# Optimization experiments

Measured on AMD Instinct MI355X. Metric: run time of the kernel, lower is better.

The kernel has to match this reference:

```python
import jax, jax.numpy as jnp
import numpy as np

D_MODEL = 1024
D_FF = 8192
N_ELEM = 64            # d2 (elements per block)
D1 = D_FF // N_ELEM    # 128 block rows
BATCH = 2048


def setup_inputs() -> dict:
    key = jax.random.key(0)
    k1, k2, k3, k4, k5 = jax.random.split(key, 5)
    # xavier-uniform-like init for w1 (d_model, d_ff) -> view (d_model, d1, d2)
    bound1 = float(np.sqrt(6.0 / (D_MODEL + D_FF)))
    w1 = jax.random.uniform(k1, (D_MODEL, D1, N_ELEM), jnp.float32, -bound1, bound1)
    # w2 (d_ff, d_model) -> view (d2, d1, d_model); kernel_scaling=True multiplies by sqrt(d2)
    w2 = jax.random.uniform(k2, (N_ELEM, D1, D_MODEL), jnp.float32, -bound1, bound1)
    w2 = w2 * (N_ELEM ** 0.5)
    b2 = jax.random.normal(k3, (D_MODEL,), jnp.float32)
    x = jax.random.normal(k4, (BATCH, D_MODEL), jnp.float32)
    quant_mask = jax.random.randint(k5, (BATCH, D1), 0, N_ELEM, jnp.int32)
    return {"quant_mask": quant_mask, "x": x, "w1": w1, "w2": w2, "b2": b2}


def reference(quant_mask, x, w1, w2, b2):
    # predict-mode path of SparseFFMain (multiply_by_controller_output=False)
    d1 = w1.shape[1]
    w1p = jnp.transpose(w1, (1, 2, 0))   # (d1, d2, d_model)
    w2p = jnp.transpose(w2, (1, 0, 2))   # (d1, d2, d_model)
    rows = jnp.arange(d1)[None, :]        # (1, d1) broadcasts over batch
    # per-sample gathered expert sub-blocks: (B, d1, d_model)
    w = w1p[rows, quant_mask]
    v = w2p[rows, quant_mask]
    mid = jnp.einsum('bd,bjd->bj', x, w)   # (B, d1)
    relu = jax.nn.relu(mid)
    res = jnp.einsum('bj,bjd->bd', relu, v) + b2  # (B, d_model)
    return (quant_mask, res)
```

## Files before the change

### kernel.cpp

```cpp
#include <hip/hip_runtime.h>

#define D_MODEL 1024
#define D_FF    8192
#define N_ELEM  64
#define D1      128
#define BATCH   2048
#define B_T     8
#define NJT     8
#define JT      16

typedef unsigned short u16;
typedef unsigned int   u32;
typedef _Float16 h2    __attribute__((ext_vector_type(2)));
typedef float    f32x4 __attribute__((ext_vector_type(4)));
typedef u32      u32x2 __attribute__((ext_vector_type(2)));
typedef u32      u32x4 __attribute__((ext_vector_type(4)));

__device__ __forceinline__ h2 as_h2(u32 u) { union { u32 i; h2 h; } c; c.i = u; return c.h; }
__device__ __forceinline__ u32 pkh(float a, float b) {
    union { h2 h; u32 u; } c; c.h.x = (_Float16)a; c.h.y = (_Float16)b; return c.u;
}
__device__ __forceinline__ u16 f2h(float f) {
    union { _Float16 h; u16 u; } c; c.h = (_Float16)f; return c.u;
}
__device__ __forceinline__ f32x4 ntload4(const float* p) {
    return __builtin_nontemporal_load((const f32x4*)p);
}
__device__ __forceinline__ float dot2(u32 a, u32 b, float c) {
#if __has_builtin(__builtin_amdgcn_fdot2)
    return __builtin_amdgcn_fdot2(as_h2(a), as_h2(b), c, false);
#else
    const h2 ha = as_h2(a), hb = as_h2(b);
    c = fmaf((float)ha.x, (float)hb.x, c);
    return fmaf((float)ha.y, (float)hb.y, c);
#endif
}
__device__ __forceinline__ float dot8(uint4 w, uint4 q, float c) {
    c = dot2(w.x, q.x, c);
    c = dot2(w.y, q.y, c);
    c = dot2(w.z, q.z, c);
    c = dot2(w.w, q.w, c);
    return c;
}

#define TW1_BLOCKS ((D_FF / 64) * (D_MODEL / 64))
__global__ __launch_bounds__(256) void prep_weights(const float* __restrict__ w1,
                                                    u16* __restrict__ w1h,
                                                    const float* __restrict__ w2,
                                                    u16* __restrict__ w2h) {
    __shared__ float tile[64][65];
    if (blockIdx.x < TW1_BLOCKS) {
        const int c0 = (blockIdx.x & (D_FF / 64 - 1)) * 64;
        const int d0 = (blockIdx.x >> 7) * 64;
        const int tx = threadIdx.x & 15;
        const int ty = threadIdx.x >> 4;
#pragma unroll
        for (int r = 0; r < 4; ++r) {
            const int row = ty * 4 + r;
            const float4 v = *(const float4*)(w1 + (size_t)(d0 + row) * D_FF + c0 + tx * 4);
            tile[row][tx * 4 + 0] = v.x;
            tile[row][tx * 4 + 1] = v.y;
            tile[row][tx * 4 + 2] = v.z;
            tile[row][tx * 4 + 3] = v.w;
        }
        __syncthreads();
#pragma unroll
        for (int r = 0; r < 4; ++r) {
            const int c = ty * 4 + r;
            ushort4 o;
            o.x = f2h(tile[tx * 4 + 0][c]);
            o.y = f2h(tile[tx * 4 + 1][c]);
            o.z = f2h(tile[tx * 4 + 2][c]);
            o.w = f2h(tile[tx * 4 + 3][c]);
            *(ushort4*)(w1h + (size_t)(c0 + c) * D_MODEL + d0 + tx * 4) = o;
        }
    } else {
        const size_t i = ((size_t)(blockIdx.x - TW1_BLOCKS) * 256 + threadIdx.x) * 8;
        const float4 a = *(const float4*)(w2 + i);
        const float4 b = *(const float4*)(w2 + i + 4);
        ushort4 oa, ob;
        oa.x = f2h(a.x); oa.y = f2h(a.y); oa.z = f2h(a.z); oa.w = f2h(a.w);
        ob.x = f2h(b.x); ob.y = f2h(b.y); ob.z = f2h(b.z); ob.w = f2h(b.w);
        *(ushort4*)(w2h + i)     = oa;
        *(ushort4*)(w2h + i + 4) = ob;
    }
}

__global__ __launch_bounds__(256) void sparse_ff_jt(const int* __restrict__ mask,
                                                    const float* __restrict__ x,
                                                    const u16* __restrict__ w1h_,
                                                    const u16* __restrict__ w2h_,
                                                    u16* __restrict__ part) {
    const _Float16* w1h = (const _Float16*)w1h_;
    const _Float16* w2h = (const _Float16*)w2h_;
    __shared__ u16   x_lds[B_T][D_MODEL];
    __shared__ float r_lds[B_T][JT];
    __shared__ int   m_lds[B_T][JT];

    const int jt = blockIdx.x & (NJT - 1);
    const int b0 = (blockIdx.x >> 3) * B_T;
    const int t = threadIdx.x;
    const int wave = t >> 6;
    const int lane = t & 63;

#pragma unroll
    for (int r = 0; r < B_T; ++r) {
        const f32x4 v = ntload4(x + (size_t)(b0 + r) * D_MODEL + t * 4);
        u32x2 o; o.x = pkh(v.x, v.y); o.y = pkh(v.z, v.w);
        *(u32x2*)&x_lds[r][t * 4] = o;
    }
    if (t < B_T * JT) {
        m_lds[t >> 4][t & 15] = mask[(b0 + (t >> 4)) * D1 + jt * JT + (t & 15)];
    }
    __syncthreads();

#pragma unroll
    for (int rep = 0; rep < 2; ++rep) {
        const int bi = wave * 2 + rep;
        const uint4 xA = *(const uint4*)&x_lds[bi][lane * 8];
        const uint4 xB = *(const uint4*)&x_lds[bi][512 + lane * 8];

#pragma unroll
        for (int jj = 0; jj < JT; jj += 4) {
            const int j0 = jt * JT + jj;
            const _Float16* c0 = w1h + (size_t)(((j0 + 0) << 6) + m_lds[bi][jj + 0]) * D_MODEL + lane * 8;
            const _Float16* c1 = w1h + (size_t)(((j0 + 1) << 6) + m_lds[bi][jj + 1]) * D_MODEL + lane * 8;
            const _Float16* c2 = w1h + (size_t)(((j0 + 2) << 6) + m_lds[bi][jj + 2]) * D_MODEL + lane * 8;
            const _Float16* c3 = w1h + (size_t)(((j0 + 3) << 6) + m_lds[bi][jj + 3]) * D_MODEL + lane * 8;
            const uint4 a0 = *(const uint4*)c0;
            const uint4 a1 = *(const uint4*)c1;
            const uint4 a2 = *(const uint4*)c2;
            const uint4 a3 = *(const uint4*)c3;
            const uint4 e0 = *(const uint4*)(c0 + 512);
            const uint4 e1 = *(const uint4*)(c1 + 512);
            const uint4 e2 = *(const uint4*)(c2 + 512);
            const uint4 e3 = *(const uint4*)(c3 + 512);

            float s0 = dot8(a0, xA, 0.f); s0 = dot8(e0, xB, s0);
            float s1 = dot8(a1, xA, 0.f); s1 = dot8(e1, xB, s1);
            float s2 = dot8(a2, xA, 0.f); s2 = dot8(e2, xB, s2);
            float s3 = dot8(a3, xA, 0.f); s3 = dot8(e3, xB, s3);

#pragma unroll
            for (int off = 32; off; off >>= 1) {
                s0 += __shfl_down(s0, off);
                s1 += __shfl_down(s1, off);
                s2 += __shfl_down(s2, off);
                s3 += __shfl_down(s3, off);
            }
            if (lane == 0) {
                r_lds[bi][jj + 0] = fmaxf(s0, 0.f);
                r_lds[bi][jj + 1] = fmaxf(s1, 0.f);
                r_lds[bi][jj + 2] = fmaxf(s2, 0.f);
                r_lds[bi][jj + 3] = fmaxf(s3, 0.f);
            }
        }
    }
    __syncthreads();

    const int halfsel = t >> 7;
    const int d0q = (t & 127) * 8;
#pragma unroll
    for (int p = 0; p < 4; ++p) {
        const int bi = p * 2 + halfsel;
        float a0 = 0.f, a1 = 0.f, a2 = 0.f, a3 = 0.f;
        float a4 = 0.f, a5 = 0.f, a6 = 0.f, a7 = 0.f;
#pragma unroll
        for (int jj = 0; jj < JT; ++jj) {
            const float r = r_lds[bi][jj];
            const _Float16* row = w2h
                + (size_t)(m_lds[bi][jj] * D1 + jt * JT + jj) * D_MODEL + d0q;
            const uint4 v = *(const uint4*)row;
            const h2 q0 = as_h2(v.x), q1 = as_h2(v.y);
            const h2 q2 = as_h2(v.z), q3 = as_h2(v.w);
            a0 = fmaf(r, (float)q0.x, a0); a1 = fmaf(r, (float)q0.y, a1);
            a2 = fmaf(r, (float)q1.x, a2); a3 = fmaf(r, (float)q1.y, a3);
            a4 = fmaf(r, (float)q2.x, a4); a5 = fmaf(r, (float)q2.y, a5);
            a6 = fmaf(r, (float)q3.x, a6); a7 = fmaf(r, (float)q3.y, a7);
        }
        u32x4 o;
        o.x = pkh(a0, a1); o.y = pkh(a2, a3);
        o.z = pkh(a4, a5); o.w = pkh(a6, a7);
        u16* pp = part + ((size_t)jt * BATCH + (b0 + bi)) * D_MODEL + d0q;
        __builtin_nontemporal_store(o, (u32x4*)pp);
    }
}

__global__ __launch_bounds__(256) void reduce_partials(const int* __restrict__ mask,
                                                       const float* __restrict__ b2,
                                                       const u16* __restrict__ part,
                                                       float* __restrict__ out) {
    const int b = blockIdx.x;
    const int t = threadIdx.x;
    if (t < D1) out[(size_t)b * D1 + t] = (float)mask[b * D1 + t];

    const int d0 = t * 4;
    const float4 bv = *(const float4*)(b2 + d0);
    float a0 = bv.x, a1 = bv.y, a2 = bv.z, a3 = bv.w;
#pragma unroll
    for (int jt = 0; jt < NJT; ++jt) {
        const uint2 v = *(const uint2*)(part + ((size_t)jt * BATCH + b) * D_MODEL + d0);
        const h2 p0 = as_h2(v.x), p1 = as_h2(v.y);
        a0 += (float)p0.x; a1 += (float)p0.y;
        a2 += (float)p1.x; a3 += (float)p1.y;
    }
    *(float4*)(out + (size_t)BATCH * D1 + (size_t)b * D_MODEL + d0) =
        make_float4(a0, a1, a2, a3);
}

__global__ __launch_bounds__(256) void sparse_ff_f32_raw(const int* __restrict__ mask,
                                                         const float* __restrict__ x,
                                                         const float* __restrict__ w1,
                                                         const float* __restrict__ w2,
                                                         const float* __restrict__ b2,
                                                         float* __restrict__ out) {
    __shared__ float x_lds[D_MODEL];
    __shared__ float relu_lds[D1];
    __shared__ int   m_lds[D1];
    const int b = blockIdx.x, t = threadIdx.x;
    const int wave = t >> 6, lane = t & 63;
    *(float4*)&x_lds[t * 4] = *(const float4*)(x + (size_t)b * D_MODEL + t * 4);
    if (t < D1) {
        const int mv = mask[b * D1 + t];
        m_lds[t] = mv;
        out[(size_t)b * D1 + t] = (float)mv;
    }
    __syncthreads();
    for (int jj = 0; jj < 32; ++jj) {
        const int j = wave * 32 + jj;
        const int m = m_lds[j];
        float acc = 0.f;
#pragma unroll
        for (int c = 0; c < 16; ++c) {
            const int d = c * 64 + lane;
            acc = fmaf(w1[(size_t)d * D_FF + j * N_ELEM + m], x_lds[d], acc);
        }
#pragma unroll
        for (int off = 32; off; off >>= 1) acc += __shfl_down(acc, off);
        if (lane == 0) relu_lds[j] = fmaxf(acc, 0.f);
    }
    __syncthreads();
    const int dm0 = t * 4;
    const float4 bv = *(const float4*)(b2 + dm0);
    float a0 = bv.x, a1 = bv.y, a2 = bv.z, a3 = bv.w;
    for (int j = 0; j < D1; ++j) {
        const float r = relu_lds[j];
        if (r > 0.f) {
            const float4 wv = *(const float4*)(w2 + (size_t)(m_lds[j] * D1 + j) * D_MODEL + dm0);
            a0 = fmaf(r, wv.x, a0); a1 = fmaf(r, wv.y, a1);
            a2 = fmaf(r, wv.z, a2); a3 = fmaf(r, wv.w, a3);
        }
    }
    *(float4*)(out + (size_t)BATCH * D1 + (size_t)b * D_MODEL + dm0) =
        make_float4(a0, a1, a2, a3);
}

extern "C" void kernel_launch(void* const* d_in, const int* in_sizes, int n_in,
                              void* d_out, int out_size, void* d_ws, size_t ws_size,
                              hipStream_t stream) {
    const int*   mask = (const int*)d_in[0];
    const float* x    = (const float*)d_in[1];
    const float* w1   = (const float*)d_in[2];
    const float* w2   = (const float*)d_in[3];
    const float* b2   = (const float*)d_in[4];
    float* out = (float*)d_out;

    const size_t w1h_bytes  = (size_t)D_FF * D_MODEL * sizeof(u16);
    const size_t w2h_bytes  = (size_t)D_FF * D_MODEL * sizeof(u16);
    const size_t part_bytes = (size_t)NJT * BATCH * D_MODEL * sizeof(u16);

    if (ws_size >= w1h_bytes + w2h_bytes + part_bytes) {
        u16* w1h  = (u16*)d_ws;
        u16* w2h  = (u16*)((char*)d_ws + w1h_bytes);
        u16* part = (u16*)((char*)d_ws + w1h_bytes + w2h_bytes);
        const int cast_blocks = (D_FF * D_MODEL / 8) / 256;
        prep_weights<<<TW1_BLOCKS + cast_blocks, 256, 0, stream>>>(w1, w1h, w2, w2h);
        sparse_ff_jt<<<(BATCH / B_T) * NJT, 256, 0, stream>>>(mask, x, w1h, w2h, part);
        reduce_partials<<<BATCH, 256, 0, stream>>>(mask, b2, part, out);
    } else {
        sparse_ff_f32_raw<<<BATCH, 256, 0, stream>>>(mask, x, w1, w2, b2, out);
    }
}
```

Measured before the change: 180.0 us.

## Fuse partial reduction into main kernel via last-block atomic counter; DPP wave reduction

Removes the separate reduce_partials launch. Each batch group of 8 j-tile blocks now increments an atomic counter, and the last block to finish sums the fp16 partials, adds the bias and writes the output. The wave-level sum switches from shuffle-down to DPP row operations that leave the result in lane 63. The second GEMV loop is split into even and odd accumulators to raise memory-level parallelism. In exchange it adds a memset, threadfences and a serialized tail on the last block of each group.

```diff
diff --git a/kernel.cpp b/kernel.cpp
--- a/kernel.cpp
+++ b/kernel.cpp
@@ -8,6 +8,7 @@
 #define B_T     8
 #define NJT     8
 #define JT      16
+#define NGRP    (BATCH / B_T)
 
 typedef unsigned short u16;
 typedef unsigned int   u32;
@@ -42,6 +43,29 @@
     c = dot2(w.w, q.w, c);
     return c;
 }
+
+#if __has_builtin(__builtin_amdgcn_update_dpp)
+#define WRITER_LANE 63
+#define DPP_ADD(x, ctrl)                                                      \
+    x += __builtin_bit_cast(float, __builtin_amdgcn_update_dpp(               \
+        0, __builtin_bit_cast(int, x), ctrl, 0xf, 0xf, true))
+__device__ __forceinline__ float wave_sum64(float x) {
+    DPP_ADD(x, 0x111);
+    DPP_ADD(x, 0x112);
+    DPP_ADD(x, 0x114);
+    DPP_ADD(x, 0x118);
+    DPP_ADD(x, 0x142);
+    DPP_ADD(x, 0x143);
+    return x;
+}
+#else
+#define WRITER_LANE 0
+__device__ __forceinline__ float wave_sum64(float x) {
+#pragma unroll
+    for (int off = 32; off; off >>= 1) x += __shfl_down(x, off);
+    return x;
+}
+#endif
 
 #define TW1_BLOCKS ((D_FF / 64) * (D_MODEL / 64))
 __global__ __launch_bounds__(256) void prep_weights(const float* __restrict__ w1,
@@ -90,12 +114,16 @@
                                                     const float* __restrict__ x,
                                                     const u16* __restrict__ w1h_,
                                                     const u16* __restrict__ w2h_,
-                                                    u16* __restrict__ part) {
+                                                    u16* part,
+                                                    int* cnt,
+                                                    const float* __restrict__ b2,
+                                                    float* __restrict__ out) {
     const _Float16* w1h = (const _Float16*)w1h_;
     const _Float16* w2h = (const _Float16*)w2h_;
     __shared__ u16   x_lds[B_T][D_MODEL];
     __shared__ float r_lds[B_T][JT];
     __shared__ int   m_lds[B_T][JT];
+    __shared__ int   last_flag;
 
     const int jt = blockIdx.x & (NJT - 1);
     const int b0 = (blockIdx.x >> 3) * B_T;
@@ -141,14 +169,11 @@
             float s2 = dot8(a2, xA, 0.f); s2 = dot8(e2, xB, s2);
             float s3 = dot8(a3, xA, 0.f); s3 = dot8(e3, xB, s3);
 
-#pragma unroll
-            for (int off = 32; off; off >>= 1) {
-                s0 += __shfl_down(s0, off);
-                s1 += __shfl_down(s1, off);
-                s2 += __shfl_down(s2, off);
-                s3 += __shfl_down(s3, off);
-            }
-            if (lane == 0) {
+            s0 = wave_sum64(s0);
+            s1 = wave_sum64(s1);
+            s2 = wave_sum64(s2);
+            s3 = wave_sum64(s3);
+            if (lane == WRITER_LANE) {
                 r_lds[bi][jj + 0] = fmaxf(s0, 0.f);
                 r_lds[bi][jj + 1] = fmaxf(s1, 0.f);
                 r_lds[bi][jj + 2] = fmaxf(s2, 0.f);
@@ -163,49 +188,72 @@
 #pragma unroll
     for (int p = 0; p < 4; ++p) {
         const int bi = p * 2 + halfsel;
-        float a0 = 0.f, a1 = 0.f, a2 = 0.f, a3 = 0.f;
-        float a4 = 0.f, a5 = 0.f, a6 = 0.f, a7 = 0.f;
-#pragma unroll
-        for (int jj = 0; jj < JT; ++jj) {
-            const float r = r_lds[bi][jj];
-            const _Float16* row = w2h
+        float e0 = 0.f, e1 = 0.f, e2 = 0.f, e3 = 0.f;
+        float e4 = 0.f, e5 = 0.f, e6 = 0.f, e7 = 0.f;
+        float o0 = 0.f, o1 = 0.f, o2 = 0.f, o3 = 0.f;
+        float o4 = 0.f, o5 = 0.f, o6 = 0.f, o7 = 0.f;
+#pragma unroll
+        for (int jj = 0; jj < JT; jj += 2) {
+            const float rE = r_lds[bi][jj];
+            const float rO = r_lds[bi][jj + 1];
+            const _Float16* rowE = w2h
                 + (size_t)(m_lds[bi][jj] * D1 + jt * JT + jj) * D_MODEL + d0q;
-            const uint4 v = *(const uint4*)row;
-            const h2 q0 = as_h2(v.x), q1 = as_h2(v.y);
-            const h2 q2 = as_h2(v.z), q3 = as_h2(v.w);
-            a0 = fmaf(r, (float)q0.x, a0); a1 = fmaf(r, (float)q0.y, a1);
-            a2 = fmaf(r, (float)q1.x, a2); a3 = fmaf(r, (float)q1.y, a3);
-            a4 = fmaf(r, (float)q2.x, a4); a5 = fmaf(r, (float)q2.y, a5);
-            a6 = fmaf(r, (float)q3.x, a6); a7 = fmaf(r, (float)q3.y, a7);
+            const _Float16* rowO = w2h
+                + (size_t)(m_lds[bi][jj + 1] * D1 + jt * JT + jj + 1) * D_MODEL + d0q;
+            const uint4 vE = *(const uint4*)rowE;
+            const uint4 vO = *(const uint4*)rowO;
+            {
+                const h2 q0 = as_h2(vE.x), q1 = as_h2(vE.y);
+                const h2 q2 = as_h2(vE.z), q3 = as_h2(vE.w);
+                e0 = fmaf(rE, (float)q0.x, e0); e1 = fmaf(rE, (float)q0.y, e1);
+                e2 = fmaf(rE, (float)q1.x, e2); e3 = fmaf(rE, (float)q1.y, e3);
+                e4 = fmaf(rE, (float)q2.x, e4); e5 = fmaf(rE, (float)q2.y, e5);
+                e6 = fmaf(rE, (float)q3.x, e6); e7 = fmaf(rE, (float)q3.y, e7);
+            }
+            {
+                const h2 q0 = as_h2(vO.x), q1 = as_h2(vO.y);
+                const h2 q2 = as_h2(vO.z), q3 = as_h2(vO.w);
+                o0 = fmaf(rO, (float)q0.x, o0); o1 = fmaf(rO, (float)q0.y, o1);
+                o2 = fmaf(rO, (float)q1.x, o2); o3 = fmaf(rO, (float)q1.y, o3);
+                o4 = fmaf(rO, (float)q2.x, o4); o5 = fmaf(rO, (float)q2.y, o5);
+                o6 = fmaf(rO, (float)q3.x, o6); o7 = fmaf(rO, (float)q3.y, o7);
+            }
         }
         u32x4 o;
-        o.x = pkh(a0, a1); o.y = pkh(a2, a3);
-        o.z = pkh(a4, a5); o.w = pkh(a6, a7);
+        o.x = pkh(e0 + o0, e1 + o1); o.y = pkh(e2 + o2, e3 + o3);
+        o.z = pkh(e4 + o4, e5 + o5); o.w = pkh(e6 + o6, e7 + o7);
         u16* pp = part + ((size_t)jt * BATCH + (b0 + bi)) * D_MODEL + d0q;
         __builtin_nontemporal_store(o, (u32x4*)pp);
     }
-}
-
-__global__ __launch_bounds__(256) void reduce_partials(const int* __restrict__ mask,
-                                                       const float* __restrict__ b2,
-                                                       const u16* __restrict__ part,
-                                                       float* __restrict__ out) {
-    const int b = blockIdx.x;
-    const int t = threadIdx.x;
-    if (t < D1) out[(size_t)b * D1 + t] = (float)mask[b * D1 + t];
-
+
+    __threadfence();
+    __syncthreads();
+    if (t == 0)
+        last_flag = (atomicAdd(&cnt[blockIdx.x >> 3], 1) == NJT - 1);
+    __syncthreads();
+    if (!last_flag) return;
+    __threadfence();
+
+    if (t < D1) {
+#pragma unroll
+        for (int bi = 0; bi < B_T; ++bi)
+            out[(size_t)(b0 + bi) * D1 + t] = (float)mask[(b0 + bi) * D1 + t];
+    }
     const int d0 = t * 4;
     const float4 bv = *(const float4*)(b2 + d0);
-    float a0 = bv.x, a1 = bv.y, a2 = bv.z, a3 = bv.w;
-#pragma unroll
-    for (int jt = 0; jt < NJT; ++jt) {
-        const uint2 v = *(const uint2*)(part + ((size_t)jt * BATCH + b) * D_MODEL + d0);
-        const h2 p0 = as_h2(v.x), p1 = as_h2(v.y);
-        a0 += (float)p0.x; a1 += (float)p0.y;
-        a2 += (float)p1.x; a3 += (float)p1.y;
-    }
-    *(float4*)(out + (size_t)BATCH * D1 + (size_t)b * D_MODEL + d0) =
-        make_float4(a0, a1, a2, a3);
+#pragma unroll
+    for (int bi = 0; bi < B_T; ++bi) {
+        float a0 = bv.x, a1 = bv.y, a2 = bv.z, a3 = bv.w;
+#pragma unroll
+        for (int q = 0; q < NJT; ++q) {
+            const uint2 v = *(const uint2*)(part + ((size_t)q * BATCH + (b0 + bi)) * D_MODEL + d0);
+            const h2 p0 = as_h2(v.x), p1 = as_h2(v.y);
+            a0 += (float)p0.x; a1 += (float)p0.y;
+            a2 += (float)p1.x; a3 += (float)p1.y;
+        }
+        *(float4*)(out + (size_t)BATCH * D1 + (size_t)(b0 + bi) * D_MODEL + d0) =
+            make_float4(a0, a1, a2, a3);
+    }
 }
 
 __global__ __launch_bounds__(256) void sparse_ff_f32_raw(const int* __restrict__ mask,
@@ -268,15 +316,18 @@
     const size_t w1h_bytes  = (size_t)D_FF * D_MODEL * sizeof(u16);
     const size_t w2h_bytes  = (size_t)D_FF * D_MODEL * sizeof(u16);
     const size_t part_bytes = (size_t)NJT * BATCH * D_MODEL * sizeof(u16);
-
-    if (ws_size >= w1h_bytes + w2h_bytes + part_bytes) {
+    const size_t cnt_bytes  = (size_t)NGRP * sizeof(int);
+
+    if (ws_size >= w1h_bytes + w2h_bytes + part_bytes + cnt_bytes) {
         u16* w1h  = (u16*)d_ws;
         u16* w2h  = (u16*)((char*)d_ws + w1h_bytes);
         u16* part = (u16*)((char*)d_ws + w1h_bytes + w2h_bytes);
+        int* cnt  = (int*)((char*)d_ws + w1h_bytes + w2h_bytes + part_bytes);
+        hipMemsetAsync(cnt, 0, cnt_bytes, stream);
         const int cast_blocks = (D_FF * D_MODEL / 8) / 256;
         prep_weights<<<TW1_BLOCKS + cast_blocks, 256, 0, stream>>>(w1, w1h, w2, w2h);
-        sparse_ff_jt<<<(BATCH / B_T) * NJT, 256, 0, stream>>>(mask, x, w1h, w2h, part);
-        reduce_partials<<<BATCH, 256, 0, stream>>>(mask, b2, part, out);
+        sparse_ff_jt<<<(BATCH / B_T) * NJT, 256, 0, stream>>>(mask, x, w1h, w2h,
+                                                              part, cnt, b2, out);
     } else {
         sparse_ff_f32_raw<<<BATCH, 256, 0, stream>>>(mask, x, w1, w2, b2, out);
     }
```

Result: slower. 690.7 us (+283.7%).

## Fuse per-wave phases with DPP wave reductions and drop LDS relu exchange

Applied to the files above, without the earlier changes.

Each wave now computes its batch rows' relu activations and keeps them in registers, then performs the second-layer accumulation for the same rows itself. This removes the r_lds shared buffer and the second __syncthreads. The shuffle-based reduction is replaced by DPP row operations plus a readlane broadcast. Each lane now handles 16 output columns instead of 8, which raises register pressure.

```diff
diff --git a/kernel.cpp b/kernel.cpp
--- a/kernel.cpp
+++ b/kernel.cpp
@@ -41,6 +41,37 @@
     c = dot2(w.z, q.z, c);
     c = dot2(w.w, q.w, c);
     return c;
+}
+
+#if __has_builtin(__builtin_amdgcn_update_dpp)
+#define WRITER_LANE 63
+#define DPP_ADD(x, ctrl)                                                      \
+    x += __builtin_bit_cast(float, __builtin_amdgcn_update_dpp(               \
+        0, __builtin_bit_cast(int, x), ctrl, 0xf, 0xf, true))
+__device__ __forceinline__ float wave_sum64(float x) {
+    DPP_ADD(x, 0x111);
+    DPP_ADD(x, 0x112);
+    DPP_ADD(x, 0x114);
+    DPP_ADD(x, 0x118);
+    DPP_ADD(x, 0x142);
+    DPP_ADD(x, 0x143);
+    return x;
+}
+#else
+#define WRITER_LANE 0
+__device__ __forceinline__ float wave_sum64(float x) {
+#pragma unroll
+    for (int off = 32; off; off >>= 1) x += __shfl_down(x, off);
+    return x;
+}
+#endif
+__device__ __forceinline__ float bcast_lane(float x, int srclane) {
+#if __has_builtin(__builtin_amdgcn_readlane)
+    return __builtin_bit_cast(float,
+        __builtin_amdgcn_readlane(__builtin_bit_cast(int, x), srclane));
+#else
+    return __shfl(x, srclane);
+#endif
 }
 
 #define TW1_BLOCKS ((D_FF / 64) * (D_MODEL / 64))
@@ -93,9 +124,8 @@
                                                     u16* __restrict__ part) {
     const _Float16* w1h = (const _Float16*)w1h_;
     const _Float16* w2h = (const _Float16*)w2h_;
-    __shared__ u16   x_lds[B_T][D_MODEL];
-    __shared__ float r_lds[B_T][JT];
-    __shared__ int   m_lds[B_T][JT];
+    __shared__ u16 x_lds[B_T][D_MODEL];
+    __shared__ int m_lds[B_T][JT];
 
     const int jt = blockIdx.x & (NJT - 1);
     const int b0 = (blockIdx.x >> 3) * B_T;
@@ -120,13 +150,20 @@
         const uint4 xA = *(const uint4*)&x_lds[bi][lane * 8];
         const uint4 xB = *(const uint4*)&x_lds[bi][512 + lane * 8];
 
+        int   mj[JT];
+        float rj[JT];
+
 #pragma unroll
         for (int jj = 0; jj < JT; jj += 4) {
+            mj[jj + 0] = m_lds[bi][jj + 0];
+            mj[jj + 1] = m_lds[bi][jj + 1];
+            mj[jj + 2] = m_lds[bi][jj + 2];
+            mj[jj + 3] = m_lds[bi][jj + 3];
             const int j0 = jt * JT + jj;
-            const _Float16* c0 = w1h + (size_t)(((j0 + 0) << 6) + m_lds[bi][jj + 0]) * D_MODEL + lane * 8;
-            const _Float16* c1 = w1h + (size_t)(((j0 + 1) << 6) + m_lds[bi][jj + 1]) * D_MODEL + lane * 8;
-            const _Float16* c2 = w1h + (size_t)(((j0 + 2) << 6) + m_lds[bi][jj + 2]) * D_MODEL + lane * 8;
-            const _Float16* c3 = w1h + (size_t)(((j0 + 3) << 6) + m_lds[bi][jj + 3]) * D_MODEL + lane * 8;
+            const _Float16* c0 = w1h + (size_t)(((j0 + 0) << 6) + mj[jj + 0]) * D_MODEL + lane * 8;
+            const _Float16* c1 = w1h + (size_t)(((j0 + 1) << 6) + mj[jj + 1]) * D_MODEL + lane * 8;
+            const _Float16* c2 = w1h + (size_t)(((j0 + 2) << 6) + mj[jj + 2]) * D_MODEL + lane * 8;
+            const _Float16* c3 = w1h + (size_t)(((j0 + 3) << 6) + mj[jj + 3]) * D_MODEL + lane * 8;
             const uint4 a0 = *(const uint4*)c0;
             const uint4 a1 = *(const uint4*)c1;
             const uint4 a2 = *(const uint4*)c2;
@@ -141,48 +178,48 @@
             float s2 = dot8(a2, xA, 0.f); s2 = dot8(e2, xB, s2);
             float s3 = dot8(a3, xA, 0.f); s3 = dot8(e3, xB, s3);
 
-#pragma unroll
-            for (int off = 32; off; off >>= 1) {
-                s0 += __shfl_down(s0, off);
-                s1 += __shfl_down(s1, off);
-                s2 += __shfl_down(s2, off);
-                s3 += __shfl_down(s3, off);
-            }
-            if (lane == 0) {
-                r_lds[bi][jj + 0] = fmaxf(s0, 0.f);
-                r_lds[bi][jj + 1] = fmaxf(s1, 0.f);
-                r_lds[bi][jj + 2] = fmaxf(s2, 0.f);
-                r_lds[bi][jj + 3] = fmaxf(s3, 0.f);
-            }
-        }
-    }
-    __syncthreads();
-
-    const int halfsel = t >> 7;
-    const int d0q = (t & 127) * 8;
-#pragma unroll
-    for (int p = 0; p < 4; ++p) {
-        const int bi = p * 2 + halfsel;
-        float a0 = 0.f, a1 = 0.f, a2 = 0.f, a3 = 0.f;
-        float a4 = 0.f, a5 = 0.f, a6 = 0.f, a7 = 0.f;
+            s0 = wave_sum64(s0);
+            s1 = wave_sum64(s1);
+            s2 = wave_sum64(s2);
+            s3 = wave_sum64(s3);
+            rj[jj + 0] = fmaxf(bcast_lane(s0, WRITER_LANE), 0.f);
+            rj[jj + 1] = fmaxf(bcast_lane(s1, WRITER_LANE), 0.f);
+            rj[jj + 2] = fmaxf(bcast_lane(s2, WRITER_LANE), 0.f);
+            rj[jj + 3] = fmaxf(bcast_lane(s3, WRITER_LANE), 0.f);
+        }
+
+        float c0 = 0.f, c1 = 0.f, c2 = 0.f, c3 = 0.f;
+        float c4 = 0.f, c5 = 0.f, c6 = 0.f, c7 = 0.f;
+        float c8 = 0.f, c9 = 0.f, cA = 0.f, cB = 0.f;
+        float cC = 0.f, cD = 0.f, cE = 0.f, cF = 0.f;
 #pragma unroll
         for (int jj = 0; jj < JT; ++jj) {
-            const float r = r_lds[bi][jj];
+            const float r = rj[jj];
             const _Float16* row = w2h
-                + (size_t)(m_lds[bi][jj] * D1 + jt * JT + jj) * D_MODEL + d0q;
-            const uint4 v = *(const uint4*)row;
-            const h2 q0 = as_h2(v.x), q1 = as_h2(v.y);
-            const h2 q2 = as_h2(v.z), q3 = as_h2(v.w);
-            a0 = fmaf(r, (float)q0.x, a0); a1 = fmaf(r, (float)q0.y, a1);
-            a2 = fmaf(r, (float)q1.x, a2); a3 = fmaf(r, (float)q1.y, a3);
-            a4 = fmaf(r, (float)q2.x, a4); a5 = fmaf(r, (float)q2.y, a5);
-            a6 = fmaf(r, (float)q3.x, a6); a7 = fmaf(r, (float)q3.y, a7);
-        }
-        u32x4 o;
-        o.x = pkh(a0, a1); o.y = pkh(a2, a3);
-        o.z = pkh(a4, a5); o.w = pkh(a6, a7);
-        u16* pp = part + ((size_t)jt * BATCH + (b0 + bi)) * D_MODEL + d0q;
-        __builtin_nontemporal_store(o, (u32x4*)pp);
+                + (size_t)(mj[jj] * D1 + jt * JT + jj) * D_MODEL + lane * 16;
+            const uint4 v0 = *(const uint4*)row;
+            const uint4 v1 = *(const uint4*)(row + 8);
+            const h2 q0 = as_h2(v0.x), q1 = as_h2(v0.y);
+            const h2 q2 = as_h2(v0.z), q3 = as_h2(v0.w);
+            const h2 q4 = as_h2(v1.x), q5 = as_h2(v1.y);
+            const h2 q6 = as_h2(v1.z), q7 = as_h2(v1.w);
+            c0 = fmaf(r, (float)q0.x, c0); c1 = fmaf(r, (float)q0.y, c1);
+            c2 = fmaf(r, (float)q1.x, c2); c3 = fmaf(r, (float)q1.y, c3);
+            c4 = fmaf(r, (float)q2.x, c4); c5 = fmaf(r, (float)q2.y, c5);
+            c6 = fmaf(r, (float)q3.x, c6); c7 = fmaf(r, (float)q3.y, c7);
+            c8 = fmaf(r, (float)q4.x, c8); c9 = fmaf(r, (float)q4.y, c9);
+            cA = fmaf(r, (float)q5.x, cA); cB = fmaf(r, (float)q5.y, cB);
+            cC = fmaf(r, (float)q6.x, cC); cD = fmaf(r, (float)q6.y, cD);
+            cE = fmaf(r, (float)q7.x, cE); cF = fmaf(r, (float)q7.y, cF);
+        }
+        u32x4 oA, oB;
+        oA.x = pkh(c0, c1); oA.y = pkh(c2, c3);
+        oA.z = pkh(c4, c5); oA.w = pkh(c6, c7);
+        oB.x = pkh(c8, c9); oB.y = pkh(cA, cB);
+        oB.z = pkh(cC, cD); oB.w = pkh(cE, cF);
+        u16* pp = part + ((size_t)jt * BATCH + (b0 + bi)) * D_MODEL + lane * 16;
+        __builtin_nontemporal_store(oA, (u32x4*)pp);
+        __builtin_nontemporal_store(oB, (u32x4*)(pp + 8));
     }
 }
 
```

Result: slower. 193.8 us (+7.7%).
